# Optimization experiments

Measured on AMD Instinct MI355X. Metric: run time of the kernel, lower is better.

The kernel has to match this reference:

```python
import jax, jax.numpy as jnp
import numpy as np

RC, RMIN = 6.0, 0.5
BETA, M1, M2 = 12, 24, 6
B, N, NT, MN = 4, 1024, 2, 128
K = NT * MN
NFEAT = M1 * M2


def _cheby(x, order):
    # Chebyshev polynomials T_0..T_{order-1} via recurrence, stacked on last axis
    Ts = [jnp.ones_like(x), x]
    for _ in range(order - 2):
        Ts.append(2.0 * x * Ts[-1] - Ts[-2])
    return jnp.stack(Ts[:order], axis=-1)


def _feat_fn(rxyz, valid, ti_map, c_param, scale):
    # rxyz: (B,N,K,3) neighbor displacement vectors; valid: (B,N,K) 0/1 float
    b, n, k, _ = rxyz.shape
    r = jnp.sqrt(jnp.sum(rxyz * rxyz, axis=-1) + 1e-12)          # (B,N,K)
    u = jnp.clip((r - RMIN) / (RC - RMIN), 0.0, 1.0)
    fc = 0.5 * (jnp.cos(jnp.pi * u) + 1.0) * valid                # smooth cutoff
    x = 2.0 * (r - RMIN) / (RC - RMIN) - 1.0
    T = _cheby(x, BETA).reshape(b, n, NT, MN, BETA)               # group slots by neighbor type
    c_i = c_param[ti_map]                                         # (N, NT, M1, BETA) gather by center type
    s = jnp.einsum('bntmk,ntfk->bntmf', T, c_i).reshape(b, n, k, M1)
    s = s * fc[..., None]                                         # (B,N,K,M1)
    inv_r = valid / r
    sr = jnp.concatenate([valid[..., None], rxyz * inv_r[..., None]], axis=-1)  # (B,N,K,4)
    R = jnp.einsum('bnkf,bnkc->bnfc', s, sr) / MN                 # (B,N,M1,4)
    feat = jnp.einsum('bnfc,bngc->bnfg', R, R[:, :, :M2]).reshape(b, n, NFEAT)
    return feat * scale


def _ei_fn(feat, ti_map, W0, b0, W1, b1, W2, b2, ener_shift):
    # evaluate all per-type fitting nets, then select by atom type
    h = jnp.tanh(jnp.einsum('bnf,tfh->bnth', feat, W0) + b0)
    h2 = jnp.tanh(jnp.einsum('bnth,thg->bntg', h, W1) + b1) + h   # resnet skip
    E = jnp.einsum('bnth,th->bnt', h2, W2) + b2 + ener_shift      # (B,N,T)
    idx = jnp.broadcast_to(ti_map[None, :, None], (E.shape[0], E.shape[1], 1))
    return jnp.take_along_axis(E, idx, axis=2)[..., 0]            # (B,N)


def setup_inputs() -> dict:
    key = jax.random.key(0)
    ks = jax.random.split(key, 16)
    num_neigh = jax.random.randint(ks[0], (B, N, NT), MN // 2, MN + 1)
    slot = jnp.arange(MN)
    vmask = slot[None, None, None, :] < num_neigh[..., None]      # (B,N,NT,MN)
    ln = jax.random.randint(ks[1], (B, N, NT, MN), 0, N)
    list_neigh = jnp.where(vmask, ln, -1)
    r = jax.random.uniform(ks[2], (B, N, K), minval=RMIN + 0.2, maxval=RC - 0.1)
    d = jax.random.normal(ks[3], (B, N, K, 3))
    d = d / jnp.linalg.norm(d, axis=-1, keepdims=True)
    rxyz = d * r[..., None]
    vm = vmask.reshape(B, N, K).astype(jnp.float32)
    ImageDR = jnp.concatenate([r[..., None], rxyz], axis=-1) * vm[..., None]
    return {
        'list_neigh': list_neigh,
        'Imagetype_map': jax.random.randint(ks[4], (N,), 0, NT),
        'atom_type': jnp.arange(NT),
        'ImageDR': ImageDR.astype(jnp.float32),
        'num_neigh': num_neigh,
        'nghost': 0,
        'c_param': jax.random.normal(ks[5], (NT, NT, M1, BETA), jnp.float32) * 0.3,
        'scale': jax.random.uniform(ks[6], (NFEAT,), jnp.float32, 0.5, 1.5),
        'W0': jax.random.normal(ks[7], (NT, NFEAT, 128), jnp.float32) * 0.08,
        'b0': jnp.zeros((NT, 128), jnp.float32),
        'W1': jax.random.normal(ks[8], (NT, 128, 128), jnp.float32) * 0.08,
        'b1': jnp.zeros((NT, 128), jnp.float32),
        'W2': jax.random.normal(ks[9], (NT, 128), jnp.float32) * 0.08,
        'b2': jnp.zeros((NT,), jnp.float32),
        'ener_shift': jax.random.normal(ks[10], (NT,), jnp.float32),
    }


def reference(list_neigh, Imagetype_map, atom_type, ImageDR, num_neigh, nghost,
              c_param, scale, W0, b0, W1, b1, W2, b2, ener_shift):
    ln = list_neigh.reshape(B, N, K)
    valid = (ln >= 0).astype(ImageDR.dtype)
    rxyz = ImageDR[..., 1:4]

    def etot(z):
        feat = _feat_fn(z, valid, Imagetype_map, c_param, scale)
        return _ei_fn(feat, Imagetype_map, W0, b0, W1, b1, W2, b2, ener_shift)

    Ei = etot(rxyz)                                               # (B,N)
    Etot = jnp.sum(Ei, axis=1)                                    # (B,)
    g = jax.grad(lambda z: etot(z).sum())(rxyz)                   # dE/dr_ij  (B,N,K,3)

    natom_tot = N + nghost
    Force = jnp.zeros((B, natom_tot, 3), ImageDR.dtype)
    Force = Force.at[:, :N].add(g.sum(axis=2))                    # center-atom contribution
    idx = jnp.where(ln >= 0, ln, natom_tot).reshape(B, N * K)     # invalid -> pad slot

    def scat(i, v):
        buf = jnp.zeros((natom_tot + 1, 3), v.dtype)
        return buf.at[i].add(v)[:natom_tot]

    Force = Force + jax.vmap(scat)(idx, (-g).reshape(B, N * K, 3))  # scatter to neighbors
    Virial = -jnp.einsum('bnkc,bnkd->bcd', rxyz, g).reshape(B, 9)
    return (Etot, Ei, Force, Virial)
```

## Files before the change

### kernel.cpp

```cpp
#include <hip/hip_runtime.h>
#include <math.h>

#define RMINF  0.5f
#define LSPAN  5.5f
constexpr int BETA = 12, M1 = 24, M2 = 6;
constexpr int B_ = 4, N_ = 1024, NT_ = 2, MN_ = 128;
constexpr int K_ = NT_ * MN_;
constexpr int NFEAT = M1 * M2;
constexpr int HID = 128;
constexpr float PI_F = 3.14159265358979323846f;

constexpr int EI_OFF = B_;
constexpr int F_OFF  = B_ + B_ * N_;
constexpr int V_OFF  = F_OFF + B_ * N_ * 3;

constexpr int G_ = 4;
constexpr int NG = B_ * N_ / G_;
constexpr int SL = 8;

constexpr size_t WS_FEAT    = 0;
constexpr size_t WS_R       = (size_t)B_ * N_ * NFEAT;
constexpr size_t WS_VIR     = WS_R + (size_t)B_ * N_ * 96;
constexpr size_t WS_CONTRIB = WS_VIR + (size_t)NG * 9;
constexpr size_t WS_PARTIAL = WS_CONTRIB + (size_t)NG * N_ * 3;


__global__ __launch_bounds__(256) void k1_embed(
    const int*   __restrict__ list_neigh,
    const int*   __restrict__ type_map,
    const float* __restrict__ imagedr,
    const float* __restrict__ c_param,
    const float* __restrict__ scale,
    float* __restrict__ feat_ws,
    float* __restrict__ R_ws)
{
    __shared__ float c_sh[NT_ * M1 * BETA];
    __shared__ float p_sh[K_][13];
    __shared__ float sr_sh[K_][5];
    __shared__ float Mpart[2][96];
    __shared__ float R_sh[96];

    const int tid = threadIdx.x;
    const int bn = blockIdx.x;
    const int n  = bn % N_;
    const int tn = type_map[n];

    for (int i = tid; i < NT_ * M1 * BETA; i += 256)
        c_sh[i] = c_param[tn * (NT_ * M1 * BETA) + i];

    const int k = tid;
    const int lni = list_neigh[(size_t)bn * K_ + k];
    const float valid = (lni >= 0) ? 1.0f : 0.0f;

    const float4 dr4 = reinterpret_cast<const float4*>(imagedr)[(size_t)bn * K_ + k];
    const float rx = dr4.y, ry = dr4.z, rz = dr4.w;
    const float r  = sqrtf(rx*rx + ry*ry + rz*rz + 1e-12f);
    const float uraw = (r - RMINF) / LSPAN;
    const float u  = fminf(fmaxf(uraw, 0.0f), 1.0f);
    const float fc = 0.5f * (cosf(PI_F * u) + 1.0f) * valid;
    const float x  = 2.0f * (r - RMINF) / LSPAN - 1.0f;

    float T[BETA];
    T[0] = 1.0f; T[1] = x;
#pragma unroll
    for (int j = 2; j < BETA; ++j) T[j] = 2.0f * x * T[j-1] - T[j-2];

    const float inv_r = 1.0f / r;
    sr_sh[k][0] = valid;
    sr_sh[k][1] = valid * rx * inv_r;
    sr_sh[k][2] = valid * ry * inv_r;
    sr_sh[k][3] = valid * rz * inv_r;
#pragma unroll
    for (int j = 0; j < BETA; ++j) p_sh[k][j] = fc * T[j];
    __syncthreads();

    if (tid < 192) {
        const int sub = tid / 96, idx = tid % 96;
        const int tk = idx / 48, rem = idx % 48;
        const int j = rem >> 2, cc = rem & 3;
        const int k0 = tk * 128 + sub * 64;
        float a0 = 0.0f, a1 = 0.0f;
        for (int kk = k0; kk < k0 + 64; kk += 2) {
            a0 = fmaf(p_sh[kk][j],   sr_sh[kk][cc],   a0);
            a1 = fmaf(p_sh[kk+1][j], sr_sh[kk+1][cc], a1);
        }
        Mpart[sub][idx] = a0 + a1;
    }
    __syncthreads();

    if (tid < 96) {
        const int f = tid >> 2, cc = tid & 3;
        float acc = 0.0f;
#pragma unroll
        for (int tk = 0; tk < NT_; ++tk) {
#pragma unroll
            for (int j = 0; j < BETA; ++j) {
                const float m = Mpart[0][tk*48 + j*4 + cc] + Mpart[1][tk*48 + j*4 + cc];
                acc = fmaf(c_sh[tk*288 + f*12 + j], m, acc);
            }
        }
        const float v = acc * (1.0f / MN_);
        R_sh[tid] = v;
        R_ws[(size_t)bn * 96 + tid] = v;
    }
    __syncthreads();
    if (tid < NFEAT) {
        const int f = tid / 6, g = tid % 6;
        float acc = 0.0f;
#pragma unroll
        for (int c = 0; c < 4; ++c) acc += R_sh[f * 4 + c] * R_sh[g * 4 + c];
        feat_ws[(size_t)bn * NFEAT + tid] = acc * scale[tid];
    }
}

__global__ __launch_bounds__(128) void k2_mlp(
    const int*   __restrict__ type_map,
    const float* __restrict__ scale,
    const float* __restrict__ W0,
    const float* __restrict__ b0,
    const float* __restrict__ W1,
    const float* __restrict__ b1,
    const float* __restrict__ W2,
    const float* __restrict__ b2,
    const float* __restrict__ eshift,
    const float* __restrict__ feat_ws,
    float* __restrict__ dfeat_ws,
    float* __restrict__ out)
{
    constexpr int WS = 145;
    __shared__ float feat_sh[4][NFEAT];
    __shared__ float h_sh[4][HID];
    __shared__ float dz1_sh[4][HID];
    __shared__ float dz0_sh[4][HID];
    __shared__ float wbuf[32 * WS];
    __shared__ float red2[4][2];

    const int tid  = threadIdx.x;
    const int c    = tid;
    const int lane = tid & 63;
    const int wv   = tid >> 6;
    const int n  = blockIdx.x;
    const int tn = type_map[n];

    for (int i = tid; i < 4 * NFEAT; i += 128) {
        const int bb = i / NFEAT, f = i % NFEAT;
        feat_sh[bb][f] = feat_ws[((size_t)bb * N_ + n) * NFEAT + f];
    }

    const float* W0t = W0 + (size_t)tn * NFEAT * HID;
    const float* W1t = W1 + (size_t)tn * HID * HID;

    float acc[4];
    {
        const float bias = b0[tn * HID + c];
        acc[0] = acc[1] = acc[2] = acc[3] = bias;
    }
    for (int ch = 0; ch < NFEAT; ch += 32) {
        const int rows = (NFEAT - ch) < 32 ? (NFEAT - ch) : 32;
        __syncthreads();
        for (int i = tid; i < rows * 128; i += 128) {
            const int f = i >> 7, cc = i & 127;
            wbuf[f * WS + cc] = W0t[(size_t)(ch + f) * HID + cc];
        }
        __syncthreads();
#pragma unroll 4
        for (int f = 0; f < rows; ++f) {
            const float w = wbuf[f * WS + c];
#pragma unroll
            for (int b = 0; b < 4; ++b)
                acc[b] = fmaf(feat_sh[b][ch + f], w, acc[b]);
        }
    }
    float hv[4];
#pragma unroll
    for (int b = 0; b < 4; ++b) { hv[b] = tanhf(acc[b]); h_sh[b][c] = hv[b]; }

    {
        const float bias = b1[tn * HID + c];
        acc[0] = acc[1] = acc[2] = acc[3] = bias;
    }
    for (int ch = 0; ch < HID; ch += 32) {
        __syncthreads();
        for (int i = tid; i < 32 * 128; i += 128) {
            const int g = i >> 7, cc = i & 127;
            wbuf[g * WS + cc] = W1t[(size_t)(ch + g) * HID + cc];
        }
        __syncthreads();
#pragma unroll 4
        for (int g = 0; g < 32; ++g) {
            const float w = wbuf[g * WS + c];
#pragma unroll
            for (int b = 0; b < 4; ++b)
                acc[b] = fmaf(h_sh[b][ch + g], w, acc[b]);
        }
    }

    const float w2c = W2[tn * HID + c];
    float ei[4];
#pragma unroll
    for (int b = 0; b < 4; ++b) {
        const float t1 = tanhf(acc[b]);
        dz1_sh[b][c] = w2c * (1.0f - t1 * t1);
        ei[b] = (t1 + hv[b]) * w2c;
    }
#pragma unroll
    for (int b = 0; b < 4; ++b) {
        float v = ei[b];
#pragma unroll
        for (int m = 32; m >= 1; m >>= 1) v += __shfl_xor(v, m);
        if (lane == 0) red2[b][wv] = v;
    }
    __syncthreads();
    if (tid < 4)
        out[EI_OFF + (size_t)tid * N_ + n] =
            red2[tid][0] + red2[tid][1] + b2[tn] + eshift[tn];

    acc[0] = acc[1] = acc[2] = acc[3] = w2c;
    for (int ch = 0; ch < HID; ch += 32) {
        __syncthreads();
        for (int i = tid; i < 32 * 128; i += 128) {
            const int j = i & 31, hh = i >> 5;
            wbuf[j * WS + hh] = W1t[(size_t)hh * HID + ch + j];
        }
        __syncthreads();
#pragma unroll 4
        for (int j = 0; j < 32; ++j) {
            const float w = wbuf[j * WS + c];
#pragma unroll
            for (int b = 0; b < 4; ++b)
                acc[b] = fmaf(dz1_sh[b][ch + j], w, acc[b]);
        }
    }
#pragma unroll
    for (int b = 0; b < 4; ++b) dz0_sh[b][c] = acc[b] * (1.0f - hv[b] * hv[b]);

    float d0[4] = {0.f, 0.f, 0.f, 0.f};
    float d1[4] = {0.f, 0.f, 0.f, 0.f};
    for (int ch = 0; ch < HID; ch += 32) {
        __syncthreads();
        for (int i = tid; i < 32 * NFEAT; i += 128) {
            const int j = i & 31, f = i >> 5;
            wbuf[j * WS + f] = W0t[(size_t)f * HID + ch + j];
        }
        __syncthreads();
#pragma unroll 4
        for (int j = 0; j < 32; ++j) {
            const float w = wbuf[j * WS + c];
            float z[4];
#pragma unroll
            for (int b = 0; b < 4; ++b) z[b] = dz0_sh[b][ch + j];
#pragma unroll
            for (int b = 0; b < 4; ++b) d0[b] = fmaf(w, z[b], d0[b]);
            if (c < NFEAT - HID) {
                const float w2 = wbuf[j * WS + HID + c];
#pragma unroll
                for (int b = 0; b < 4; ++b) d1[b] = fmaf(w2, z[b], d1[b]);
            }
        }
    }
    {
        const float sc = scale[c];
#pragma unroll
        for (int b = 0; b < 4; ++b)
            dfeat_ws[((size_t)b * N_ + n) * NFEAT + c] = d0[b] * sc;
        if (c < NFEAT - HID) {
            const float sc2 = scale[HID + c];
#pragma unroll
            for (int b = 0; b < 4; ++b)
                dfeat_ws[((size_t)b * N_ + n) * NFEAT + HID + c] = d1[b] * sc2;
        }
    }
}

__global__ __launch_bounds__(256) void k3_bwd(
    const int*   __restrict__ list_neigh,
    const int*   __restrict__ type_map,
    const float* __restrict__ imagedr,
    const float* __restrict__ c_param,
    const float* __restrict__ dfeat_ws,
    const float* __restrict__ R_ws,
    float* __restrict__ contrib_ws,
    float* __restrict__ vir_ws)
{
    __shared__ float fcontrib[N_ * 3];
    __shared__ float c_sh[NT_ * M1 * BETA];
    __shared__ float dfeat_sh[NFEAT];
    __shared__ float R_sh[96];
    __shared__ float dR_sh[96];
    __shared__ float A_sh[96];
    __shared__ float red12[12 * 4];

    const int tid  = threadIdx.x;
    const int lane = tid & 63;
    const int wid  = tid >> 6;
    const int g  = blockIdx.x;
    const int tk = tid >> 7;

    for (int i = tid; i < N_ * 3; i += 256) fcontrib[i] = 0.0f;

    float vv0=0.f,vv1=0.f,vv2=0.f,vv3=0.f,vv4=0.f,vv5=0.f,vv6=0.f,vv7=0.f,vv8=0.f;

    for (int aa = 0; aa < G_; ++aa) {
        const int bn = g * G_ + aa;
        const int n  = bn & (N_ - 1);
        const int tn = type_map[n];

        __syncthreads();
        for (int i = tid; i < NT_ * M1 * BETA; i += 256)
            c_sh[i] = c_param[tn * (NT_ * M1 * BETA) + i];
        if (tid < NFEAT) dfeat_sh[tid] = dfeat_ws[(size_t)bn * NFEAT + tid];
        if (tid < 96)    R_sh[tid]     = R_ws[(size_t)bn * 96 + tid];
        __syncthreads();

        if (tid < 96) {
            const int p = tid >> 2, c = tid & 3;
            float acc = 0.0f;
#pragma unroll
            for (int gg = 0; gg < M2; ++gg) acc += dfeat_sh[p * 6 + gg] * R_sh[gg * 4 + c];
            if (p < M2) {
                for (int f = 0; f < M1; ++f) acc += dfeat_sh[f * 6 + p] * R_sh[f * 4 + c];
            }
            dR_sh[p * 4 + c] = acc * (1.0f / MN_);
        }
        __syncthreads();

        if (tid < 96) {
            const int atk = tid / 48, rem = tid % 48;
            const int j = rem >> 2, cc = rem & 3;
            float acc = 0.0f;
#pragma unroll
            for (int f = 0; f < M1; ++f)
                acc = fmaf(c_sh[atk*288 + f*12 + j], dR_sh[f*4 + cc], acc);
            A_sh[tid] = acc;
        }
        __syncthreads();

        const int lni = list_neigh[(size_t)bn * K_ + tid];
        const float valid = (lni >= 0) ? 1.0f : 0.0f;
        const float4 dr4 = reinterpret_cast<const float4*>(imagedr)[(size_t)bn * K_ + tid];
        const float rx = dr4.y, ry = dr4.z, rz = dr4.w;
        const float r  = sqrtf(rx*rx + ry*ry + rz*rz + 1e-12f);
        const float uraw = (r - RMINF) / LSPAN;
        const float u  = fminf(fmaxf(uraw, 0.0f), 1.0f);
        const float fc = 0.5f * (cosf(PI_F * u) + 1.0f) * valid;
        const float x  = 2.0f * (r - RMINF) / LSPAN - 1.0f;

        float T[BETA];
        T[0] = 1.0f; T[1] = x;
#pragma unroll
        for (int j = 2; j < BETA; ++j) T[j] = 2.0f * x * T[j-1] - T[j-2];

        const float inv_r = 1.0f / r;
        const float sr0 = valid;
        const float sr1 = valid * rx * inv_r;
        const float sr2 = valid * ry * inv_r;
        const float sr3 = valid * rz * inv_r;

        const float* Arow = &A_sh[tk * 48];
        float dfc = 0.0f, dx = 0.0f;
        float tA0 = 0.0f, tA1 = 0.0f, tA2 = 0.0f, tA3 = 0.0f;
        float tpm1 = 1.0f, tpm2 = 0.0f;
#pragma unroll
        for (int j = 0; j < BETA; ++j) {
            const float a0 = Arow[j*4+0], a1 = Arow[j*4+1];
            const float a2 = Arow[j*4+2], a3 = Arow[j*4+3];
            const float cjj = a0*sr0 + a1*sr1 + a2*sr2 + a3*sr3;
            dfc = fmaf(T[j], cjj, dfc);
            tA0 = fmaf(T[j], a0, tA0);
            tA1 = fmaf(T[j], a1, tA1);
            tA2 = fmaf(T[j], a2, tA2);
            tA3 = fmaf(T[j], a3, tA3);
            if (j == 1) {
                dx = cjj;
            } else if (j >= 2) {
                const float tp = 2.0f * T[j-1] + 2.0f * x * tpm1 - tpm2;
                dx = fmaf(cjj, tp, dx);
                tpm2 = tpm1; tpm1 = tp;
            }
        }
        const float dsr1 = fc * tA1, dsr2 = fc * tA2, dsr3 = fc * tA3;

        float dfcdr = 0.0f;
        if (uraw > 0.0f && uraw < 1.0f)
            dfcdr = -0.5f * PI_F * sinf(PI_F * u) * valid / LSPAN;
        const float drt = (fc * dx) * (2.0f / LSPAN) + dfc * dfcdr;
        const float Sdot = dsr1 * rx + dsr2 * ry + dsr3 * rz;
        const float common = drt * inv_r - valid * Sdot * inv_r * inv_r * inv_r;
        const float gx = common * rx + valid * dsr1 * inv_r;
        const float gy = common * ry + valid * dsr2 * inv_r;
        const float gz = common * rz + valid * dsr3 * inv_r;

        if (lni >= 0) {
            atomicAdd(&fcontrib[lni * 3 + 0], -gx);
            atomicAdd(&fcontrib[lni * 3 + 1], -gy);
            atomicAdd(&fcontrib[lni * 3 + 2], -gz);
        }

        {
            float s0 = gx, s1 = gy, s2 = gz;
#pragma unroll
            for (int m = 32; m >= 1; m >>= 1) {
                s0 += __shfl_xor(s0, m);
                s1 += __shfl_xor(s1, m);
                s2 += __shfl_xor(s2, m);
            }
            if (lane == 0) {
                red12[0 * 4 + wid] = s0;
                red12[1 * 4 + wid] = s1;
                red12[2 * 4 + wid] = s2;
            }
        }
        __syncthreads();
        if (tid < 3) {
            const float v = red12[tid*4+0] + red12[tid*4+1] + red12[tid*4+2] + red12[tid*4+3];
            atomicAdd(&fcontrib[n * 3 + tid], v);
        }

        vv0 = fmaf(-rx, gx, vv0); vv1 = fmaf(-rx, gy, vv1); vv2 = fmaf(-rx, gz, vv2);
        vv3 = fmaf(-ry, gx, vv3); vv4 = fmaf(-ry, gy, vv4); vv5 = fmaf(-ry, gz, vv5);
        vv6 = fmaf(-rz, gx, vv6); vv7 = fmaf(-rz, gy, vv7); vv8 = fmaf(-rz, gz, vv8);
    }

    {
        float vals[9] = {vv0,vv1,vv2,vv3,vv4,vv5,vv6,vv7,vv8};
        __syncthreads();
#pragma unroll
        for (int i = 0; i < 9; ++i) {
            float v = vals[i];
#pragma unroll
            for (int m = 32; m >= 1; m >>= 1) v += __shfl_xor(v, m);
            if (lane == 0) red12[i * 4 + wid] = v;
        }
        __syncthreads();
        if (tid < 9)
            vir_ws[(size_t)g * 9 + tid] = red12[tid*4+0] + red12[tid*4+1]
                                        + red12[tid*4+2] + red12[tid*4+3];
    }

    __syncthreads();
    {
        float4* dst = reinterpret_cast<float4*>(contrib_ws + (size_t)g * (N_ * 3));
        const float4* src = reinterpret_cast<const float4*>(fcontrib);
        for (int i = tid; i < (N_ * 3) / 4; i += 256) dst[i] = src[i];
    }
}

__global__ __launch_bounds__(256) void k3_reduce(
    const float* __restrict__ contrib_ws,
    float* __restrict__ partial_ws)
{
    const int x  = blockIdx.x;
    const int ch = x % 3;
    const int bb = (x / 3) % B_;
    const int s  = x / (3 * B_);
    const int c4 = ch * 256 + threadIdx.x;
    const int rows = (NG / B_) / SL;
    const int g0 = bb * (NG / B_) + s * rows;

    const float4* src = reinterpret_cast<const float4*>(contrib_ws);
    float4 a0 = {0,0,0,0}, a1 = {0,0,0,0};
    for (int r = 0; r < rows; r += 2) {
        const float4 v0 = src[(size_t)(g0 + r)     * 768 + c4];
        const float4 v1 = src[(size_t)(g0 + r + 1) * 768 + c4];
        a0.x += v0.x; a0.y += v0.y; a0.z += v0.z; a0.w += v0.w;
        a1.x += v1.x; a1.y += v1.y; a1.z += v1.z; a1.w += v1.w;
    }
    const float4 res = {a0.x + a1.x, a0.y + a1.y, a0.z + a1.z, a0.w + a1.w};
    reinterpret_cast<float4*>(partial_ws)[(size_t)(s * B_ + bb) * 768 + c4] = res;
}

__global__ __launch_bounds__(256) void k4_final(
    const float* __restrict__ vir_ws,
    const float* __restrict__ partial_ws,
    float* __restrict__ out)
{
    __shared__ float red[10 * 4];
    const int tid  = threadIdx.x;
    const int lane = tid & 63;
    const int wid  = tid >> 6;
    const int b = blockIdx.x;

    for (int i = tid; i < N_ * 3; i += 256) {
        float f = 0.0f;
#pragma unroll
        for (int s = 0; s < SL; ++s) f += partial_ws[(size_t)(s * B_ + b) * (N_ * 3) + i];
        out[F_OFF + (size_t)b * (N_ * 3) + i] = f;
    }

    float vals[10];
#pragma unroll
    for (int i = 0; i < 10; ++i) vals[i] = 0.0f;
    for (int n = tid; n < N_; n += 256) vals[0] += out[EI_OFF + b * N_ + n];
    {
        const float* vp = vir_ws + ((size_t)b * (NG / B_) + tid) * 9;
#pragma unroll
        for (int j = 0; j < 9; ++j) vals[1 + j] = vp[j];
    }
#pragma unroll
    for (int i = 0; i < 10; ++i) {
        float v = vals[i];
#pragma unroll
        for (int m = 32; m >= 1; m >>= 1) v += __shfl_xor(v, m);
        if (lane == 0) red[i * 4 + wid] = v;
    }
    __syncthreads();
    if (tid < 10) {
        const float v = red[tid*4+0] + red[tid*4+1] + red[tid*4+2] + red[tid*4+3];
        if (tid == 0) out[b] = v;
        else          out[V_OFF + b * 9 + (tid - 1)] = v;
    }
}

extern "C" void kernel_launch(void* const* d_in, const int* in_sizes, int n_in,
                              void* d_out, int out_size, void* d_ws, size_t ws_size,
                              hipStream_t stream) {
    float* out = (float*)d_out;
    float* ws  = (float*)d_ws;
    float* feat_ws    = ws + WS_FEAT;
    float* R_ws       = ws + WS_R;
    float* vir_ws     = ws + WS_VIR;
    float* contrib_ws = ws + WS_CONTRIB;
    float* partial_ws = ws + WS_PARTIAL;

    const int*   list_neigh = (const int*)d_in[0];
    const int*   type_map   = (const int*)d_in[1];
    const float* imagedr    = (const float*)d_in[3];
    const float* c_param    = (const float*)d_in[6];
    const float* scale      = (const float*)d_in[7];
    const float* W0 = (const float*)d_in[8];
    const float* b0 = (const float*)d_in[9];
    const float* W1 = (const float*)d_in[10];
    const float* b1 = (const float*)d_in[11];
    const float* W2 = (const float*)d_in[12];
    const float* b2 = (const float*)d_in[13];
    const float* eshift = (const float*)d_in[14];

    k1_embed<<<B_ * N_, 256, 0, stream>>>(list_neigh, type_map, imagedr, c_param,
                                          scale, feat_ws, R_ws);
    k2_mlp<<<N_, 128, 0, stream>>>(type_map, scale, W0, b0, W1, b1, W2, b2,
                                   eshift, feat_ws, feat_ws , out);
    k3_bwd<<<NG, 256, 0, stream>>>(list_neigh, type_map, imagedr, c_param,
                                   feat_ws , R_ws, contrib_ws, vir_ws);
    k3_reduce<<<SL * B_ * 3, 256, 0, stream>>>(contrib_ws, partial_ws);
    k4_final<<<B_, 256, 0, stream>>>(vir_ws, partial_ws, out);
}
```

Measured before the change: 207.6 us.

## Batch MLP by atom type and split backward prep into separate kernel

A new sort kernel groups atoms by type into tiles of four, so each MLP block processes 16 rows (4 atoms × 4 batches) that share one set of weights. This amortizes the per-block weight staging across more rows and uses 256 threads. The per-atom dR/A computation moves out of the backward kernel into its own prep kernel, which lets the backward kernel handle 8 atoms per block and halves the number of contribution rows to reduce. The cost is two extra launches, extra workspace traffic for A, and padded tiles when a type count is not a multiple of four.

New measurement: 202.3 us. 1.03x faster.

```diff
diff --git a/kernel.cpp b/kernel.cpp
--- a/kernel.cpp
+++ b/kernel.cpp
@@ -14,16 +14,39 @@
 constexpr int F_OFF  = B_ + B_ * N_;
 constexpr int V_OFF  = F_OFF + B_ * N_ * 3;
 
-constexpr int G_ = 4;
-constexpr int NG = B_ * N_ / G_;
+constexpr int G3 = 8;
+constexpr int NG3 = B_ * N_ / G3;
 constexpr int SL = 8;
+constexpr int NTILE = 258;
 
 constexpr size_t WS_FEAT    = 0;
 constexpr size_t WS_R       = (size_t)B_ * N_ * NFEAT;
-constexpr size_t WS_VIR     = WS_R + (size_t)B_ * N_ * 96;
-constexpr size_t WS_CONTRIB = WS_VIR + (size_t)NG * 9;
-constexpr size_t WS_PARTIAL = WS_CONTRIB + (size_t)NG * N_ * 3;
-
+constexpr size_t WS_A       = WS_R + (size_t)B_ * N_ * 96;
+constexpr size_t WS_VIR     = WS_A + (size_t)B_ * N_ * 96;
+constexpr size_t WS_CONTRIB = WS_VIR + (size_t)NG3 * 9;
+constexpr size_t WS_PARTIAL = WS_CONTRIB + (size_t)NG3 * N_ * 3;
+constexpr size_t WS_SITES   = WS_PARTIAL + (size_t)SL * B_ * N_ * 3;
+
+
+__global__ void k0_sort(const int* __restrict__ type_map, int* __restrict__ sites)
+{
+    __shared__ int counts[2];
+    __shared__ int base[2];
+    __shared__ int cursor[2];
+    const int tid = threadIdx.x;
+    if (tid < 2) { counts[tid] = 0; cursor[tid] = 0; }
+    for (int i = tid; i < NTILE * 4; i += 1024) sites[i] = -1;
+    __syncthreads();
+    int myt = -1;
+    if (tid < N_) { myt = type_map[tid]; atomicAdd(&counts[myt], 1); }
+    __syncthreads();
+    if (tid == 0) { base[0] = 0; base[1] = ((counts[0] + 3) >> 2) << 2; }
+    __syncthreads();
+    if (tid < N_) {
+        const int p = atomicAdd(&cursor[myt], 1);
+        sites[base[myt] + p] = tid;
+    }
+}
 
 __global__ __launch_bounds__(256) void k1_embed(
     const int*   __restrict__ list_neigh,
@@ -113,7 +136,7 @@
     }
 }
 
-__global__ __launch_bounds__(128) void k2_mlp(
+__global__ __launch_bounds__(256) void k2_mlp(
     const int*   __restrict__ type_map,
     const float* __restrict__ scale,
     const float* __restrict__ W0,
@@ -125,168 +148,248 @@
     const float* __restrict__ eshift,
     const float* __restrict__ feat_ws,
     float* __restrict__ dfeat_ws,
-    float* __restrict__ out)
+    float* __restrict__ out,
+    const int* __restrict__ sites)
 {
-    constexpr int WS = 145;
-    __shared__ float feat_sh[4][NFEAT];
-    __shared__ float h_sh[4][HID];
-    __shared__ float dz1_sh[4][HID];
-    __shared__ float dz0_sh[4][HID];
-    __shared__ float wbuf[32 * WS];
-    __shared__ float red2[4][2];
+    constexpr int WSR = 145;
+    __shared__ float feat2[NFEAT * 20];
+    __shared__ float h2[HID * 20];
+    __shared__ float dz1_2[HID * 20];
+    __shared__ float dz0_2[HID * 20];
+    __shared__ float wbuf[32 * WSR];
+    __shared__ float red[4][8];
+    __shared__ int   s_sh[4];
 
     const int tid  = threadIdx.x;
-    const int c    = tid;
+    const int c    = tid & 127;
+    const int half = tid >> 7;
     const int lane = tid & 63;
-    const int wv   = tid >> 6;
-    const int n  = blockIdx.x;
-    const int tn = type_map[n];
-
-    for (int i = tid; i < 4 * NFEAT; i += 128) {
-        const int bb = i / NFEAT, f = i % NFEAT;
-        feat_sh[bb][f] = feat_ws[((size_t)bb * N_ + n) * NFEAT + f];
+    const int wid  = tid >> 6;
+
+    if (tid < 4) s_sh[tid] = sites[blockIdx.x * 4 + tid];
+    __syncthreads();
+    int sarr[4];
+#pragma unroll
+    for (int i = 0; i < 4; ++i) sarr[i] = s_sh[i];
+    const int sv = sarr[0] >= 0 ? sarr[0] : (sarr[1] >= 0 ? sarr[1]
+                 : (sarr[2] >= 0 ? sarr[2] : sarr[3]));
+    if (sv < 0) return;
+    const int tn = type_map[sv];
+
+    for (int r = 0; r < 16; ++r) {
+        const int si = r >> 2, bb = r & 3;
+        const int s = sarr[si];
+        if (tid < NFEAT)
+            feat2[tid * 20 + r] = (s >= 0)
+                ? feat_ws[((size_t)bb * N_ + s) * NFEAT + tid] : 0.0f;
     }
 
     const float* W0t = W0 + (size_t)tn * NFEAT * HID;
     const float* W1t = W1 + (size_t)tn * HID * HID;
 
-    float acc[4];
+    float acc[8];
     {
         const float bias = b0[tn * HID + c];
-        acc[0] = acc[1] = acc[2] = acc[3] = bias;
+#pragma unroll
+        for (int a = 0; a < 8; ++a) acc[a] = bias;
     }
     for (int ch = 0; ch < NFEAT; ch += 32) {
         const int rows = (NFEAT - ch) < 32 ? (NFEAT - ch) : 32;
         __syncthreads();
-        for (int i = tid; i < rows * 128; i += 128) {
+        for (int i = tid; i < rows * 128; i += 256) {
             const int f = i >> 7, cc = i & 127;
-            wbuf[f * WS + cc] = W0t[(size_t)(ch + f) * HID + cc];
+            wbuf[f * WSR + cc] = W0t[(size_t)(ch + f) * HID + cc];
         }
         __syncthreads();
 #pragma unroll 4
-        for (int f = 0; f < rows; ++f) {
-            const float w = wbuf[f * WS + c];
-#pragma unroll
-            for (int b = 0; b < 4; ++b)
-                acc[b] = fmaf(feat_sh[b][ch + f], w, acc[b]);
-        }
-    }
-    float hv[4];
-#pragma unroll
-    for (int b = 0; b < 4; ++b) { hv[b] = tanhf(acc[b]); h_sh[b][c] = hv[b]; }
+        for (int f0 = 0; f0 < rows; ++f0) {
+            const float w = wbuf[f0 * WSR + c];
+            const float4 fa = *reinterpret_cast<const float4*>(&feat2[(ch+f0)*20 + half*8]);
+            const float4 fb = *reinterpret_cast<const float4*>(&feat2[(ch+f0)*20 + half*8 + 4]);
+            acc[0] = fmaf(fa.x, w, acc[0]); acc[1] = fmaf(fa.y, w, acc[1]);
+            acc[2] = fmaf(fa.z, w, acc[2]); acc[3] = fmaf(fa.w, w, acc[3]);
+            acc[4] = fmaf(fb.x, w, acc[4]); acc[5] = fmaf(fb.y, w, acc[5]);
+            acc[6] = fmaf(fb.z, w, acc[6]); acc[7] = fmaf(fb.w, w, acc[7]);
+        }
+    }
+    float hv[8];
+#pragma unroll
+    for (int a = 0; a < 8; ++a) {
+        hv[a] = tanhf(acc[a]);
+        h2[c * 20 + half * 8 + a] = hv[a];
+    }
 
     {
         const float bias = b1[tn * HID + c];
-        acc[0] = acc[1] = acc[2] = acc[3] = bias;
+#pragma unroll
+        for (int a = 0; a < 8; ++a) acc[a] = bias;
     }
     for (int ch = 0; ch < HID; ch += 32) {
         __syncthreads();
-        for (int i = tid; i < 32 * 128; i += 128) {
+        for (int i = tid; i < 32 * 128; i += 256) {
             const int g = i >> 7, cc = i & 127;
-            wbuf[g * WS + cc] = W1t[(size_t)(ch + g) * HID + cc];
+            wbuf[g * WSR + cc] = W1t[(size_t)(ch + g) * HID + cc];
         }
         __syncthreads();
 #pragma unroll 4
-        for (int g = 0; g < 32; ++g) {
-            const float w = wbuf[g * WS + c];
-#pragma unroll
-            for (int b = 0; b < 4; ++b)
-                acc[b] = fmaf(h_sh[b][ch + g], w, acc[b]);
+        for (int g0 = 0; g0 < 32; ++g0) {
+            const float w = wbuf[g0 * WSR + c];
+            const float4 ha = *reinterpret_cast<const float4*>(&h2[(ch+g0)*20 + half*8]);
+            const float4 hb = *reinterpret_cast<const float4*>(&h2[(ch+g0)*20 + half*8 + 4]);
+            acc[0] = fmaf(ha.x, w, acc[0]); acc[1] = fmaf(ha.y, w, acc[1]);
+            acc[2] = fmaf(ha.z, w, acc[2]); acc[3] = fmaf(ha.w, w, acc[3]);
+            acc[4] = fmaf(hb.x, w, acc[4]); acc[5] = fmaf(hb.y, w, acc[5]);
+            acc[6] = fmaf(hb.z, w, acc[6]); acc[7] = fmaf(hb.w, w, acc[7]);
         }
     }
 
     const float w2c = W2[tn * HID + c];
-    float ei[4];
-#pragma unroll
-    for (int b = 0; b < 4; ++b) {
-        const float t1 = tanhf(acc[b]);
-        dz1_sh[b][c] = w2c * (1.0f - t1 * t1);
-        ei[b] = (t1 + hv[b]) * w2c;
-    }
-#pragma unroll
-    for (int b = 0; b < 4; ++b) {
-        float v = ei[b];
+    float ei[8];
+#pragma unroll
+    for (int a = 0; a < 8; ++a) {
+        const float t1 = tanhf(acc[a]);
+        dz1_2[c * 20 + half * 8 + a] = w2c * (1.0f - t1 * t1);
+        ei[a] = (t1 + hv[a]) * w2c;
+    }
+#pragma unroll
+    for (int a = 0; a < 8; ++a) {
+        float v = ei[a];
 #pragma unroll
         for (int m = 32; m >= 1; m >>= 1) v += __shfl_xor(v, m);
-        if (lane == 0) red2[b][wv] = v;
-    }
-    __syncthreads();
-    if (tid < 4)
-        out[EI_OFF + (size_t)tid * N_ + n] =
-            red2[tid][0] + red2[tid][1] + b2[tn] + eshift[tn];
-
-    acc[0] = acc[1] = acc[2] = acc[3] = w2c;
+        if (lane == 0) red[wid][a] = v;
+    }
+    __syncthreads();
+    if (tid < 16) {
+        const int hh = tid >> 3, a = tid & 7;
+        const int si = tid >> 2, bb = tid & 3;
+        const int s = sarr[si];
+        if (s >= 0)
+            out[EI_OFF + (size_t)bb * N_ + s] =
+                red[hh*2][a] + red[hh*2+1][a] + b2[tn] + eshift[tn];
+    }
+
+#pragma unroll
+    for (int a = 0; a < 8; ++a) acc[a] = w2c;
     for (int ch = 0; ch < HID; ch += 32) {
         __syncthreads();
-        for (int i = tid; i < 32 * 128; i += 128) {
+        for (int i = tid; i < 32 * 128; i += 256) {
             const int j = i & 31, hh = i >> 5;
-            wbuf[j * WS + hh] = W1t[(size_t)hh * HID + ch + j];
+            wbuf[j * WSR + hh] = W1t[(size_t)hh * HID + ch + j];
         }
         __syncthreads();
 #pragma unroll 4
         for (int j = 0; j < 32; ++j) {
-            const float w = wbuf[j * WS + c];
-#pragma unroll
-            for (int b = 0; b < 4; ++b)
-                acc[b] = fmaf(dz1_sh[b][ch + j], w, acc[b]);
-        }
-    }
-#pragma unroll
-    for (int b = 0; b < 4; ++b) dz0_sh[b][c] = acc[b] * (1.0f - hv[b] * hv[b]);
-
-    float d0[4] = {0.f, 0.f, 0.f, 0.f};
-    float d1[4] = {0.f, 0.f, 0.f, 0.f};
+            const float w = wbuf[j * WSR + c];
+            const float4 za = *reinterpret_cast<const float4*>(&dz1_2[(ch+j)*20 + half*8]);
+            const float4 zb = *reinterpret_cast<const float4*>(&dz1_2[(ch+j)*20 + half*8 + 4]);
+            acc[0] = fmaf(za.x, w, acc[0]); acc[1] = fmaf(za.y, w, acc[1]);
+            acc[2] = fmaf(za.z, w, acc[2]); acc[3] = fmaf(za.w, w, acc[3]);
+            acc[4] = fmaf(zb.x, w, acc[4]); acc[5] = fmaf(zb.y, w, acc[5]);
+            acc[6] = fmaf(zb.z, w, acc[6]); acc[7] = fmaf(zb.w, w, acc[7]);
+        }
+    }
+#pragma unroll
+    for (int a = 0; a < 8; ++a)
+        dz0_2[c * 20 + half * 8 + a] = acc[a] * (1.0f - hv[a] * hv[a]);
+
+    float d0[8] = {0,0,0,0,0,0,0,0};
+    float d1[8] = {0,0,0,0,0,0,0,0};
+    const int c2 = (c < NFEAT - HID) ? (HID + c) : HID;
     for (int ch = 0; ch < HID; ch += 32) {
         __syncthreads();
-        for (int i = tid; i < 32 * NFEAT; i += 128) {
+        for (int i = tid; i < 32 * NFEAT; i += 256) {
             const int j = i & 31, f = i >> 5;
-            wbuf[j * WS + f] = W0t[(size_t)f * HID + ch + j];
+            wbuf[j * WSR + f] = W0t[(size_t)f * HID + ch + j];
         }
         __syncthreads();
 #pragma unroll 4
         for (int j = 0; j < 32; ++j) {
-            const float w = wbuf[j * WS + c];
-            float z[4];
-#pragma unroll
-            for (int b = 0; b < 4; ++b) z[b] = dz0_sh[b][ch + j];
-#pragma unroll
-            for (int b = 0; b < 4; ++b) d0[b] = fmaf(w, z[b], d0[b]);
-            if (c < NFEAT - HID) {
-                const float w2 = wbuf[j * WS + HID + c];
-#pragma unroll
-                for (int b = 0; b < 4; ++b) d1[b] = fmaf(w2, z[b], d1[b]);
+            const float w  = wbuf[j * WSR + c];
+            const float w2 = wbuf[j * WSR + c2];
+            const float4 za = *reinterpret_cast<const float4*>(&dz0_2[(ch+j)*20 + half*8]);
+            const float4 zb = *reinterpret_cast<const float4*>(&dz0_2[(ch+j)*20 + half*8 + 4]);
+            d0[0] = fmaf(za.x, w, d0[0]); d0[1] = fmaf(za.y, w, d0[1]);
+            d0[2] = fmaf(za.z, w, d0[2]); d0[3] = fmaf(za.w, w, d0[3]);
+            d0[4] = fmaf(zb.x, w, d0[4]); d0[5] = fmaf(zb.y, w, d0[5]);
+            d0[6] = fmaf(zb.z, w, d0[6]); d0[7] = fmaf(zb.w, w, d0[7]);
+            d1[0] = fmaf(za.x, w2, d1[0]); d1[1] = fmaf(za.y, w2, d1[1]);
+            d1[2] = fmaf(za.z, w2, d1[2]); d1[3] = fmaf(za.w, w2, d1[3]);
+            d1[4] = fmaf(zb.x, w2, d1[4]); d1[5] = fmaf(zb.y, w2, d1[5]);
+            d1[6] = fmaf(zb.z, w2, d1[6]); d1[7] = fmaf(zb.w, w2, d1[7]);
+        }
+    }
+    {
+        const float sc  = scale[c];
+        const float sc2 = (c < NFEAT - HID) ? scale[HID + c] : 0.0f;
+#pragma unroll
+        for (int a = 0; a < 8; ++a) {
+            const int r = half * 8 + a;
+            const int si = r >> 2, bb = r & 3;
+            const int s = sarr[si];
+            if (s >= 0) {
+                dfeat_ws[((size_t)bb * N_ + s) * NFEAT + c] = d0[a] * sc;
+                if (c < NFEAT - HID)
+                    dfeat_ws[((size_t)bb * N_ + s) * NFEAT + HID + c] = d1[a] * sc2;
             }
         }
     }
-    {
-        const float sc = scale[c];
-#pragma unroll
-        for (int b = 0; b < 4; ++b)
-            dfeat_ws[((size_t)b * N_ + n) * NFEAT + c] = d0[b] * sc;
-        if (c < NFEAT - HID) {
-            const float sc2 = scale[HID + c];
-#pragma unroll
-            for (int b = 0; b < 4; ++b)
-                dfeat_ws[((size_t)b * N_ + n) * NFEAT + HID + c] = d1[b] * sc2;
-        }
-    }
-}
-
-__global__ __launch_bounds__(256) void k3_bwd(
-    const int*   __restrict__ list_neigh,
+}
+
+__global__ __launch_bounds__(256) void k3a_prep(
     const int*   __restrict__ type_map,
-    const float* __restrict__ imagedr,
     const float* __restrict__ c_param,
     const float* __restrict__ dfeat_ws,
     const float* __restrict__ R_ws,
+    float* __restrict__ A_ws)
+{
+    __shared__ float call[NT_ * NT_ * M1 * BETA];
+    __shared__ float df[2][NFEAT];
+    __shared__ float R2[2][96];
+    __shared__ float dR2[2][96];
+
+    const int tid = threadIdx.x;
+    const int bn0 = blockIdx.x * 2;
+
+    for (int i = tid; i < NT_ * NT_ * M1 * BETA; i += 256) call[i] = c_param[i];
+    for (int i = tid; i < 2 * NFEAT; i += 256)
+        df[i / NFEAT][i % NFEAT] = dfeat_ws[(size_t)(bn0 + i / NFEAT) * NFEAT + i % NFEAT];
+    for (int i = tid; i < 2 * 96; i += 256)
+        R2[i / 96][i % 96] = R_ws[(size_t)(bn0 + i / 96) * 96 + i % 96];
+    __syncthreads();
+
+    if (tid < 192) {
+        const int at = tid / 96, idx = tid % 96;
+        const int p = idx >> 2, cc = idx & 3;
+        float a = 0.0f;
+#pragma unroll
+        for (int gg = 0; gg < M2; ++gg) a += df[at][p * 6 + gg] * R2[at][gg * 4 + cc];
+        if (p < M2) {
+            for (int f = 0; f < M1; ++f) a += df[at][f * 6 + p] * R2[at][f * 4 + cc];
+        }
+        dR2[at][idx] = a * (1.0f / MN_);
+    }
+    __syncthreads();
+    if (tid < 192) {
+        const int at = tid / 96, idx = tid % 96;
+        const int tkk = idx / 48, rem = idx % 48;
+        const int j = rem >> 2, cc = rem & 3;
+        const int tnat = type_map[(bn0 + at) & (N_ - 1)];
+        float a = 0.0f;
+#pragma unroll
+        for (int f = 0; f < M1; ++f)
+            a = fmaf(call[tnat * 576 + tkk * 288 + f * 12 + j], dR2[at][f * 4 + cc], a);
+        A_ws[(size_t)(bn0 + at) * 96 + idx] = a;
+    }
+}
+
+__global__ __launch_bounds__(256) void k3_bwd(
+    const int*   __restrict__ list_neigh,
+    const float* __restrict__ imagedr,
+    const float* __restrict__ A_ws,
     float* __restrict__ contrib_ws,
     float* __restrict__ vir_ws)
 {
     __shared__ float fcontrib[N_ * 3];
-    __shared__ float c_sh[NT_ * M1 * BETA];
-    __shared__ float dfeat_sh[NFEAT];
-    __shared__ float R_sh[96];
-    __shared__ float dR_sh[96];
     __shared__ float A_sh[96];
     __shared__ float red12[12 * 4];
 
@@ -300,39 +403,12 @@
 
     float vv0=0.f,vv1=0.f,vv2=0.f,vv3=0.f,vv4=0.f,vv5=0.f,vv6=0.f,vv7=0.f,vv8=0.f;
 
-    for (int aa = 0; aa < G_; ++aa) {
-        const int bn = g * G_ + aa;
+    for (int aa = 0; aa < G3; ++aa) {
+        const int bn = g * G3 + aa;
         const int n  = bn & (N_ - 1);
-        const int tn = type_map[n];
-
-        __syncthreads();
-        for (int i = tid; i < NT_ * M1 * BETA; i += 256)
-            c_sh[i] = c_param[tn * (NT_ * M1 * BETA) + i];
-        if (tid < NFEAT) dfeat_sh[tid] = dfeat_ws[(size_t)bn * NFEAT + tid];
-        if (tid < 96)    R_sh[tid]     = R_ws[(size_t)bn * 96 + tid];
-        __syncthreads();
-
-        if (tid < 96) {
-            const int p = tid >> 2, c = tid & 3;
-            float acc = 0.0f;
-#pragma unroll
-            for (int gg = 0; gg < M2; ++gg) acc += dfeat_sh[p * 6 + gg] * R_sh[gg * 4 + c];
-            if (p < M2) {
-                for (int f = 0; f < M1; ++f) acc += dfeat_sh[f * 6 + p] * R_sh[f * 4 + c];
-            }
-            dR_sh[p * 4 + c] = acc * (1.0f / MN_);
-        }
-        __syncthreads();
-
-        if (tid < 96) {
-            const int atk = tid / 48, rem = tid % 48;
-            const int j = rem >> 2, cc = rem & 3;
-            float acc = 0.0f;
-#pragma unroll
-            for (int f = 0; f < M1; ++f)
-                acc = fmaf(c_sh[atk*288 + f*12 + j], dR_sh[f*4 + cc], acc);
-            A_sh[tid] = acc;
-        }
+
+        __syncthreads();
+        if (tid < 96) A_sh[tid] = A_ws[(size_t)bn * 96 + tid];
         __syncthreads();
 
         const int lni = list_neigh[(size_t)bn * K_ + tid];
@@ -358,7 +434,7 @@
 
         const float* Arow = &A_sh[tk * 48];
         float dfc = 0.0f, dx = 0.0f;
-        float tA0 = 0.0f, tA1 = 0.0f, tA2 = 0.0f, tA3 = 0.0f;
+        float tA1 = 0.0f, tA2 = 0.0f, tA3 = 0.0f;
         float tpm1 = 1.0f, tpm2 = 0.0f;
 #pragma unroll
         for (int j = 0; j < BETA; ++j) {
@@ -366,7 +442,6 @@
             const float a2 = Arow[j*4+2], a3 = Arow[j*4+3];
             const float cjj = a0*sr0 + a1*sr1 + a2*sr2 + a3*sr3;
             dfc = fmaf(T[j], cjj, dfc);
-            tA0 = fmaf(T[j], a0, tA0);
             tA1 = fmaf(T[j], a1, tA1);
             tA2 = fmaf(T[j], a2, tA2);
             tA3 = fmaf(T[j], a3, tA3);
@@ -454,8 +529,8 @@
     const int bb = (x / 3) % B_;
     const int s  = x / (3 * B_);
     const int c4 = ch * 256 + threadIdx.x;
-    const int rows = (NG / B_) / SL;
-    const int g0 = bb * (NG / B_) + s * rows;
+    const int rows = (NG3 / B_) / SL;
+    const int g0 = bb * (NG3 / B_) + s * rows;
 
     const float4* src = reinterpret_cast<const float4*>(contrib_ws);
     float4 a0 = {0,0,0,0}, a1 = {0,0,0,0};
@@ -491,8 +566,8 @@
 #pragma unroll
     for (int i = 0; i < 10; ++i) vals[i] = 0.0f;
     for (int n = tid; n < N_; n += 256) vals[0] += out[EI_OFF + b * N_ + n];
-    {
-        const float* vp = vir_ws + ((size_t)b * (NG / B_) + tid) * 9;
+    if (tid < NG3 / B_) {
+        const float* vp = vir_ws + ((size_t)b * (NG3 / B_) + tid) * 9;
 #pragma unroll
         for (int j = 0; j < 9; ++j) vals[1 + j] = vp[j];
     }
@@ -518,9 +593,11 @@
     float* ws  = (float*)d_ws;
     float* feat_ws    = ws + WS_FEAT;
     float* R_ws       = ws + WS_R;
+    float* A_ws       = ws + WS_A;
     float* vir_ws     = ws + WS_VIR;
     float* contrib_ws = ws + WS_CONTRIB;
     float* partial_ws = ws + WS_PARTIAL;
+    int*   sites_ws   = (int*)(ws + WS_SITES);
 
     const int*   list_neigh = (const int*)d_in[0];
     const int*   type_map   = (const int*)d_in[1];
@@ -535,12 +612,15 @@
     const float* b2 = (const float*)d_in[13];
     const float* eshift = (const float*)d_in[14];
 
+    k0_sort<<<1, 1024, 0, stream>>>(type_map, sites_ws);
     k1_embed<<<B_ * N_, 256, 0, stream>>>(list_neigh, type_map, imagedr, c_param,
                                           scale, feat_ws, R_ws);
-    k2_mlp<<<N_, 128, 0, stream>>>(type_map, scale, W0, b0, W1, b1, W2, b2,
-                                   eshift, feat_ws, feat_ws , out);
-    k3_bwd<<<NG, 256, 0, stream>>>(list_neigh, type_map, imagedr, c_param,
-                                   feat_ws , R_ws, contrib_ws, vir_ws);
+    k2_mlp<<<NTILE, 256, 0, stream>>>(type_map, scale, W0, b0, W1, b1, W2, b2,
+                                      eshift, feat_ws, feat_ws , out,
+                                      sites_ws);
+    k3a_prep<<<B_ * N_ / 2, 256, 0, stream>>>(type_map, c_param, feat_ws ,
+                                              R_ws, A_ws);
+    k3_bwd<<<NG3, 256, 0, stream>>>(list_neigh, imagedr, A_ws, contrib_ws, vir_ws);
     k3_reduce<<<SL * B_ * 3, 256, 0, stream>>>(contrib_ws, partial_ws);
     k4_final<<<B_, 256, 0, stream>>>(vir_ws, partial_ws, out);
 }
```
